# Kernel tuning notes

Measured on AMD Instinct MI355X. Metric: run time of the kernel, lower is better.

## Reference

```python
import jax, jax.numpy as jnp
import numpy as np

SAMPLE_POINTS = 1000
THRESH = 0.1
MAX_RATIO = 0.1
BIG = 1e9


def _sobel_boundary(mask):
    # mask: [B, H, W] -> boundary magnitude [B, H, W]
    kx = jnp.array([[-1, 0, 1], [-2, 0, 2], [-1, 0, 1]], jnp.float32).reshape(1, 1, 3, 3)
    ky = jnp.array([[-1, -2, -1], [0, 0, 0], [1, 2, 1]], jnp.float32).reshape(1, 1, 3, 3)
    x = mask[:, None, :, :]
    dn = ('NCHW', 'OIHW', 'NCHW')
    gx = jax.lax.conv_general_dilated(x, kx, (1, 1), [(1, 1), (1, 1)], dimension_numbers=dn)
    gy = jax.lax.conv_general_dilated(x, ky, (1, 1), [(1, 1), (1, 1)], dimension_numbers=dn)
    return jnp.sqrt(gx * gx + gy * gy + 1e-8)[:, 0]


def _extract_points(bmap, keys, H, W):
    # bmap: [B, H, W]. Returns points [B, P, 2] float and validity mask [B, P].
    # Torch version uses torch.where + randperm subsampling; here we pick a
    # uniformly-random subset of valid boundary pixels via noisy top_k
    # (fixed-shape, jit-compatible stream compaction).
    def one(bm, key):
        flat = bm.reshape(-1)
        valid = flat > THRESH
        noise = jax.random.uniform(key, flat.shape)
        score = valid.astype(jnp.float32) * 2.0 + noise  # valid in (2,3), invalid in (0,1)
        _, idx = jax.lax.top_k(score, SAMPLE_POINTS)
        pts = jnp.stack([(idx // W).astype(jnp.float32), (idx % W).astype(jnp.float32)], axis=-1)
        pvalid = valid[idx]
        has_any = valid.any()
        # empty-boundary fallback: single center point (like torch version)
        center = jnp.array([H // 2, W // 2], jnp.float32)
        pts = jnp.where(has_any, pts, jnp.broadcast_to(center, pts.shape))
        pvalid = jnp.where(has_any, pvalid, jnp.arange(SAMPLE_POINTS) == 0)
        return pts, pvalid

    return jax.vmap(one)(bmap, keys)


def _hausdorff(pp, pv, tp, tv, diag):
    # pp: [B,P,2], tp: [B,T,2]; masked symmetric Hausdorff per batch element.
    pp2 = jnp.sum(pp * pp, -1)  # [B,P]
    tp2 = jnp.sum(tp * tp, -1)  # [B,T]
    d2 = pp2[:, :, None] + tp2[:, None, :] - 2.0 * jnp.einsum('bpc,btc->bpt', pp, tp)
    D = jnp.sqrt(jnp.maximum(d2, 0.0))  # [B,P,T]
    min_p2t = jnp.min(jnp.where(tv[:, None, :], D, BIG), axis=2)  # [B,P]
    a = jnp.max(jnp.where(pv, min_p2t, -BIG), axis=1)  # [B]
    min_t2p = jnp.min(jnp.where(pv[:, :, None], D, BIG), axis=1)  # [B,T]
    b = jnp.max(jnp.where(tv, min_t2p, -BIG), axis=1)  # [B]
    hd = jnp.maximum(a, b) / diag
    return jnp.clip(hd, 0.0, MAX_RATIO)


def setup_inputs() -> dict:
    key = jax.random.key(0)
    k1, k2 = jax.random.split(key)
    B, H, W = 64, 512, 512
    pred_logits = jax.random.normal(k1, (B, H, W), dtype=jnp.float32)
    target = (jax.random.uniform(k2, (B, H, W)) > 0.5).astype(jnp.float32)
    return {"pred_logits": pred_logits, "target": target}


def reference(pred_logits, target):
    B, H, W = pred_logits.shape
    pred_probs = jax.nn.sigmoid(pred_logits)
    bmap_pred = _sobel_boundary(pred_probs)
    bmap_tgt = _sobel_boundary(target)
    keys = jax.random.split(jax.random.key(1), 2 * B)
    pp, pv = _extract_points(bmap_pred, keys[:B], H, W)
    tp, tv = _extract_points(bmap_tgt, keys[B:], H, W)
    diag = jnp.sqrt(jnp.float32(H * H + W * W))
    hd = _hausdorff(pp, pv, tp, tv, diag)  # [B]
    return jnp.mean(hd)
```

## Files before the change

### kernel.cpp

```cpp
#include <hip/hip_runtime.h>
#include <stdint.h>


#define HH 512
#define WW 512
#define NPIX (HH * WW)
#define NSEL 1000
#define SLICE_CAP 320
#define CUTM (253u << 14)
#define BITCUT ((((253u << 15) - 1u)) << 9)
#define ROWS_PER 32

#if __has_builtin(__builtin_amdgcn_alignbit)
__device__ __forceinline__ uint32_t rotl32(uint32_t x, int r) {
  return __builtin_amdgcn_alignbit(x, x, (32 - r) & 31);
}
#else
__device__ __forceinline__ uint32_t rotl32(uint32_t x, int r) {
  return (x << r) | (x >> (32 - r));
}
#endif

__device__ __forceinline__ void tf2x32(uint32_t k0, uint32_t k1,
                                       uint32_t c0, uint32_t c1,
                                       uint32_t& o0, uint32_t& o1) {
  uint32_t ks2 = k0 ^ k1 ^ 0x1BD11BDAu;
  uint32_t x0 = c0 + k0, x1 = c1 + k1;
#define TF_R(r) { x0 += x1; x1 = rotl32(x1, (r)); x1 ^= x0; }
  TF_R(13) TF_R(15) TF_R(26) TF_R(6)
  x0 += k1;  x1 += ks2 + 1u;
  TF_R(17) TF_R(29) TF_R(16) TF_R(24)
  x0 += ks2; x1 += k0 + 2u;
  TF_R(13) TF_R(15) TF_R(26) TF_R(6)
  x0 += k0;  x1 += k1 + 3u;
  TF_R(17) TF_R(29) TF_R(16) TF_R(24)
  x0 += k1;  x1 += ks2 + 4u;
  TF_R(13) TF_R(15) TF_R(26) TF_R(6)
  x0 += ks2; x1 += k0 + 5u;
#undef TF_R
  o0 = x0; o1 = x1;
}

__device__ __forceinline__ uint32_t tf_bits(uint32_t k0, uint32_t k1, uint32_t p) {
  uint32_t ks2 = k0 ^ k1 ^ 0x1BD11BDAu;
  uint32_t x0 = k0, x1 = p + k1;
#define TF_R(r) { x0 += x1; x1 = rotl32(x1, (r)); x1 ^= x0; }
  TF_R(13) TF_R(15) TF_R(26) TF_R(6)
  x0 += k1;  x1 += ks2 + 1u;
  TF_R(17) TF_R(29) TF_R(16) TF_R(24)
  x0 += ks2; x1 += k0 + 2u;
  TF_R(13) TF_R(15) TF_R(26) TF_R(6)
  x0 += k0;  x1 += k1 + 3u;
  TF_R(17) TF_R(29) TF_R(16) TF_R(24)
  x0 += k1;  x1 += ks2 + 4u;
  TF_R(13) TF_R(15) TF_R(26) TF_R(6)
  x0 += ks2; x1 += k0 + 5u;
#undef TF_R
  return x0 ^ x1;
}

__device__ __forceinline__ uint32_t m_from_bits(uint32_t bits) {
  float noise = __uint_as_float((bits >> 9) | 0x3F800000u) - 1.0f;
  float score = 2.0f + noise;
  return __float_as_uint(score) - 0x40000000u;
}

__device__ __forceinline__ uint32_t pixel_m(uint32_t k0, uint32_t k1, int p) {
  uint32_t b1, b2;
  tf2x32(k0, k1, 0u, (uint32_t)p, b1, b2);
  return m_from_bits(b1 ^ b2);
}

__device__ __forceinline__ float sigf(float x) { return 1.0f / (1.0f + __expf(-x)); }

__device__ __forceinline__ float ldval(const float* __restrict__ img, int r, int c, bool isPred) {
  if (r < 0 || r > HH - 1 || c < 0 || c > WW - 1) return 0.0f;
  float v = img[(size_t)r * WW + c];
  return isPred ? sigf(v) : v;
}

__device__ __forceinline__ uint32_t pack_pt(uint32_t p) {
  return ((p >> 9) << 16) | (p & 511u);
}

template <bool PRED>
__device__ __forceinline__ void load_row10(const float* __restrict__ img, int rn,
                                           int lane, float v[10]) {
  if ((unsigned)rn < (unsigned)HH) {
    const float* rp = img + ((size_t)rn << 9) + (lane << 3);
    float4 x = *(const float4*)rp;
    float4 y = *(const float4*)(rp + 4);
    if (PRED) {
      x.x = sigf(x.x); x.y = sigf(x.y); x.z = sigf(x.z); x.w = sigf(x.w);
      y.x = sigf(y.x); y.y = sigf(y.y); y.z = sigf(y.z); y.w = sigf(y.w);
    }
    v[1] = x.x; v[2] = x.y; v[3] = x.z; v[4] = x.w;
    v[5] = y.x; v[6] = y.y; v[7] = y.z; v[8] = y.w;
    float l = __shfl_up(y.w, 1);
    float r = __shfl_down(x.x, 1);
    v[0] = (lane == 0) ? 0.0f : l;
    v[9] = (lane == 63) ? 0.0f : r;
  } else {
#pragma unroll
    for (int i = 0; i < 10; ++i) v[i] = 0.0f;
  }
}

template <bool PRED>
__device__ __forceinline__ void sobel_body(const float* __restrict__ img, int b,
                                           int slice, int t,
                                           unsigned long long* stage, int* s_cn,
                                           int* s_cv) {
  const int lane = t & 63, w = t >> 6;
  const int rbase = slice * ROWS_PER + 8 * w;
  uint32_t k0, k1;
  tf2x32(0u, 1u, 0u, (uint32_t)b, k0, k1);

  float A[10], B_[10], C_[10], D_[10], E_[10], F_[10];
  load_row10<PRED>(img, rbase - 1, lane, A);
  load_row10<PRED>(img, rbase, lane, B_);

  int cnt = 0;
  uint32_t prow = (uint32_t)((rbase << 9) + (lane << 3));

  auto do_row = [&](const float (&P)[10], const float (&Q)[10], const float (&R)[10],
                    uint32_t prow_r) {
    uint32_t bits[8];
#pragma unroll
    for (int j = 0; j < 8; ++j) bits[j] = tf_bits(k0, k1, prow_r + (uint32_t)j);
    float da[10], e[10];
#pragma unroll
    for (int k = 0; k < 10; ++k) {
      da[k] = R[k] - P[k];
      e[k] = P[k] + 2.0f * Q[k] + R[k];
    }
    uint32_t vldmask = 0, candmask = 0;
#pragma unroll
    for (int j = 0; j < 8; ++j) {
      float gx = e[j + 2] - e[j];
      float gy = da[j] + 2.0f * da[j + 1] + da[j + 2];
      bool vld = (gx * gx + gy * gy + 1e-8f) > 0.01f;
      vldmask |= (vld ? 1u : 0u) << j;
      candmask |= ((vld && bits[j] >= BITCUT) ? 1u : 0u) << j;
    }
    cnt += __popc(vldmask);
    while (candmask) {
      int j = __ffs(candmask) - 1;
      candmask &= candmask - 1;
      uint32_t m = m_from_bits(bits[j]);
      int i = atomicAdd(s_cn, 1);
      if (i < SLICE_CAP)
        stage[i] = ((unsigned long long)m << 32) | (prow_r + (uint32_t)j);
    }
  };

#pragma unroll
  for (int g = 0; g < 2; ++g) {
    const int r = rbase + 4 * g;
    load_row10<PRED>(img, r + 1, lane, C_);
    load_row10<PRED>(img, r + 2, lane, D_);
    load_row10<PRED>(img, r + 3, lane, E_);
    load_row10<PRED>(img, r + 4, lane, F_);
    do_row(A, B_, C_, prow);
    do_row(B_, C_, D_, prow + 512);
    do_row(C_, D_, E_, prow + 1024);
    do_row(D_, E_, F_, prow + 1536);
    if (g == 0) {
#pragma unroll
      for (int k = 0; k < 10; ++k) { A[k] = E_[k]; B_[k] = F_[k]; }
      prow += 2048;
    }
  }
#pragma unroll
  for (int o = 32; o > 0; o >>= 1) cnt += __shfl_down(cnt, o);
  if (lane == 0) atomicAdd(s_cv, cnt);
}

__global__ __launch_bounds__(256, 4) void sobel_cand(
    const float* __restrict__ pred, const float* __restrict__ tgt,
    int2* __restrict__ g_scnt, unsigned long long* __restrict__ g_cand) {
  const int bid = blockIdx.x;
  const int b = bid >> 4, s = bid & 15;
  const int t = threadIdx.x;
  __shared__ unsigned long long stage[SLICE_CAP];
  __shared__ int s_cn, s_cv;
  if (t == 0) { s_cn = 0; s_cv = 0; }
  __syncthreads();
  if (b < 64) sobel_body<true>(pred + (size_t)b * NPIX, b, s, t, stage, &s_cn, &s_cv);
  else        sobel_body<false>(tgt + (size_t)(b - 64) * NPIX, b, s, t, stage, &s_cn, &s_cv);
  __syncthreads();
  const int raw = s_cn;
  const int n = raw < SLICE_CAP ? raw : SLICE_CAP;
  for (int i = t; i < n; i += 256) g_cand[(size_t)bid * SLICE_CAP + i] = stage[i];
  if (t == 0) g_scnt[bid] = make_int2(s_cv, raw);
}

__global__ __launch_bounds__(256) void resolve_kernel(
    const float* __restrict__ pred, const float* __restrict__ tgt,
    const int2* __restrict__ g_scnt, unsigned long long* __restrict__ g_cand,
    uint32_t* __restrict__ g_pts, int* __restrict__ g_counts) {
  const int img = blockIdx.x;
  const int t = threadIdx.x;

  __shared__ int segc[16];
  __shared__ int s_info[4];
  __shared__ int ch[256];
  __shared__ int fh[1024];
  __shared__ int aux[256];
  __shared__ unsigned long long ties[256];
  __shared__ int s_pos, s_nt, s_T1, s_r1, s_T2, s_r2;

  if (t == 0) {
    int cv = 0, hi = 0, ovf = 0;
    for (int s = 0; s < 16; ++s) {
      int2 v = g_scnt[img * 16 + s];
      cv += v.x;
      hi += v.y;
      segc[s] = v.y < SLICE_CAP ? v.y : SLICE_CAP;
      if (v.y > SLICE_CAP) ovf = 1;
    }
    s_info[0] = cv; s_info[1] = hi; s_info[2] = ovf;
    s_pos = 0; s_nt = 0;
  }
  __syncthreads();
  const int cv = s_info[0];
  if (cv == 0) {
    if (t == 0) { g_pts[img * NSEL] = (256u << 16) | 256u; g_counts[img] = 1; }
    return;
  }
  const int need = cv < NSEL ? cv : NSEL;
  bool slow = (s_info[2] != 0) || (s_info[1] < need);

  unsigned long long* C = g_cand + (size_t)img * 16 * SLICE_CAP;
  int ncand;

  if (slow) {
    const bool isPred = img < 64;
    const float* im = isPred ? pred + (size_t)img * NPIX : tgt + (size_t)(img - 64) * NPIX;
    uint32_t k0, k1;
    tf2x32(0u, 1u, 0u, (uint32_t)img, k0, k1);
    ch[t] = 0;
    __syncthreads();
    for (int p = t; p < NPIX; p += 256) {
      int r = p >> 9, c = p & 511;
      float gx = (ldval(im, r - 1, c + 1, isPred) - ldval(im, r - 1, c - 1, isPred)) +
                 2.0f * (ldval(im, r, c + 1, isPred) - ldval(im, r, c - 1, isPred)) +
                 (ldval(im, r + 1, c + 1, isPred) - ldval(im, r + 1, c - 1, isPred));
      float gy = (ldval(im, r + 1, c - 1, isPred) - ldval(im, r - 1, c - 1, isPred)) +
                 2.0f * (ldval(im, r + 1, c, isPred) - ldval(im, r - 1, c, isPred)) +
                 (ldval(im, r + 1, c + 1, isPred) - ldval(im, r - 1, c + 1, isPred));
      if ((gx * gx + gy * gy + 1e-8f) > 0.01f) {
        uint32_t m = pixel_m(k0, k1, p);
        uint32_t cb = m >> 14; if (cb > 255u) cb = 255u;
        atomicAdd(&ch[cb], 1);
      }
    }
    __syncthreads();
    {
      aux[t] = ch[t];
      __syncthreads();
      for (int o = 1; o < 256; o <<= 1) {
        int v = (t + o < 256) ? aux[t + o] : 0;
        __syncthreads();
        aux[t] += v;
        __syncthreads();
      }
      int nx = (t + 1 < 256) ? aux[t + 1] : 0;
      if (aux[t] >= need && nx < need) s_T1 = t;
      __syncthreads();
    }
    const uint32_t Tc = (uint32_t)s_T1;
    if (t == 0) s_info[3] = 0;
    __syncthreads();
    for (int p = t; p < NPIX; p += 256) {
      int r = p >> 9, c = p & 511;
      float gx = (ldval(im, r - 1, c + 1, isPred) - ldval(im, r - 1, c - 1, isPred)) +
                 2.0f * (ldval(im, r, c + 1, isPred) - ldval(im, r, c - 1, isPred)) +
                 (ldval(im, r + 1, c + 1, isPred) - ldval(im, r + 1, c - 1, isPred));
      float gy = (ldval(im, r + 1, c - 1, isPred) - ldval(im, r - 1, c - 1, isPred)) +
                 2.0f * (ldval(im, r + 1, c, isPred) - ldval(im, r - 1, c, isPred)) +
                 (ldval(im, r + 1, c + 1, isPred) - ldval(im, r - 1, c + 1, isPred));
      if ((gx * gx + gy * gy + 1e-8f) > 0.01f) {
        uint32_t m = pixel_m(k0, k1, p);
        uint32_t cb = m >> 14; if (cb > 255u) cb = 255u;
        if (cb >= Tc) {
          int i = atomicAdd(&s_info[3], 1);
          if (i < 16 * SLICE_CAP) C[i] = ((unsigned long long)m << 32) | (uint32_t)p;
        }
      }
    }
    __syncthreads();
    ncand = s_info[3] < 16 * SLICE_CAP ? s_info[3] : 16 * SLICE_CAP;
    if (t == 0) { segc[0] = ncand; for (int s = 1; s < 16; ++s) segc[s] = 0; }
    __syncthreads();
  }

  ch[t] = 0;
  for (int i = t; i < 1024; i += 256) fh[i] = 0;
  __syncthreads();
  for (int s = 0; s < 16; ++s) {
    const unsigned long long* seg = C + (size_t)s * SLICE_CAP;
    for (int i = t; i < segc[s]; i += 256) {
      uint32_t m = (uint32_t)(seg[i] >> 32);
      uint32_t cb = m >> 14; if (cb > 255u) cb = 255u;
      atomicAdd(&ch[cb], 1);
    }
  }
  __syncthreads();
  {
    aux[t] = ch[t];
    __syncthreads();
    for (int o = 1; o < 256; o <<= 1) {
      int v = (t + o < 256) ? aux[t + o] : 0;
      __syncthreads();
      aux[t] += v;
      __syncthreads();
    }
    int nx = (t + 1 < 256) ? aux[t + 1] : 0;
    if (aux[t] >= need && nx < need) { s_T1 = t; s_r1 = need - nx; }
    __syncthreads();
  }
  const uint32_t T1 = (uint32_t)s_T1;
  const int r1 = s_r1;
  const uint32_t baseM = T1 << 14;

  for (int s = 0; s < 16; ++s) {
    const unsigned long long* seg = C + (size_t)s * SLICE_CAP;
    for (int i = t; i < segc[s]; i += 256) {
      unsigned long long e = seg[i];
      uint32_t m = (uint32_t)(e >> 32), p = (uint32_t)e;
      uint32_t cb = m >> 14; if (cb > 255u) cb = 255u;
      if (cb > T1) {
        int pos = atomicAdd(&s_pos, 1);
        g_pts[img * NSEL + pos] = pack_pt(p);
      } else if (cb == T1) {
        uint32_t f = (m - baseM) >> 4; if (f > 1023u) f = 1023u;
        atomicAdd(&fh[f], 1);
      }
    }
  }
  __syncthreads();
  {
    int base = 4 * t, sv = 0;
    for (int j = 3; j >= 0; --j) { sv += fh[base + j]; fh[base + j] = sv; }
    aux[t] = sv;
    __syncthreads();
    for (int o = 1; o < 256; o <<= 1) {
      int v = (t + o < 256) ? aux[t + o] : 0;
      __syncthreads();
      aux[t] += v;
      __syncthreads();
    }
    int add = (t < 255) ? aux[t + 1] : 0;
    for (int j = 0; j < 4; ++j) fh[base + j] += add;
    __syncthreads();
    for (int j = 0; j < 4; ++j) {
      int idx = base + j;
      int sfx = fh[idx];
      int nx = (idx < 1023) ? fh[idx + 1] : 0;
      if (sfx >= r1 && nx < r1) { s_T2 = idx; s_r2 = r1 - nx; }
    }
    __syncthreads();
  }
  const int T2 = s_T2, r2 = s_r2;
  for (int s = 0; s < 16; ++s) {
    const unsigned long long* seg = C + (size_t)s * SLICE_CAP;
    for (int i = t; i < segc[s]; i += 256) {
      unsigned long long e = seg[i];
      uint32_t m = (uint32_t)(e >> 32), p = (uint32_t)e;
      uint32_t cb = m >> 14; if (cb > 255u) cb = 255u;
      if (cb == T1) {
        uint32_t f = (m - baseM) >> 4; if (f > 1023u) f = 1023u;
        if ((int)f > T2) {
          int pos = atomicAdd(&s_pos, 1);
          g_pts[img * NSEL + pos] = pack_pt(p);
        } else if ((int)f == T2) {
          int j = atomicAdd(&s_nt, 1);
          if (j < 256) ties[j] = e;
        }
      }
    }
  }
  __syncthreads();
  int nt = s_nt < 256 ? s_nt : 256;
  for (int i = t; i < nt; i += 256) {
    unsigned long long e = ties[i];
    uint32_t mi = (uint32_t)(e >> 32), pi = (uint32_t)e;
    int rank = 0;
    for (int j = 0; j < nt; ++j) {
      unsigned long long e2 = ties[j];
      uint32_t mj = (uint32_t)(e2 >> 32), pj = (uint32_t)e2;
      rank += (mj > mi) || (mj == mi && pj < pi);
    }
    if (rank < r2) {
      int pos = atomicAdd(&s_pos, 1);
      g_pts[img * NSEL + pos] = pack_pt(pi);
    }
  }
  __syncthreads();
  if (t == 0) g_counts[img] = s_pos;
}

__global__ __launch_bounds__(256) void haus_kernel(
    const uint32_t* __restrict__ g_pts, const int* __restrict__ g_counts,
    float* __restrict__ g_hpart) {
  const int bid = blockIdx.x;
  const int img = bid >> 3;
  const int dir = (bid >> 2) & 1;
  const int seg = bid & 3;
  const int t = threadIdx.x;
  const int iOwn = dir ? 64 + img : img;
  const int iOth = dir ? img : 64 + img;
  const int nOwn = g_counts[iOwn];
  const int nOth = g_counts[iOth];
  __shared__ float2 o[NSEL];
  __shared__ float red[256];
  for (int i = t; i < nOth; i += 256) {
    uint32_t v = g_pts[iOth * NSEL + i];
    o[i] = make_float2((float)(v >> 16), (float)(v & 0xFFFFu));
  }
  __syncthreads();
  float best = 0.0f;
  const int lo = seg * 250;
  const int hi = min(nOwn, lo + 250);
  for (int i = lo + t; i < hi; i += 256) {
    uint32_t v = g_pts[iOwn * NSEL + i];
    float pr = (float)(v >> 16), pc = (float)(v & 0xFFFFu);
    float mn0 = 3.4e38f, mn1 = 3.4e38f, mn2 = 3.4e38f, mn3 = 3.4e38f;
    int j = 0;
    for (; j + 3 < nOth; j += 4) {
      float dr0 = pr - o[j].x,     dc0 = pc - o[j].y;
      float dr1 = pr - o[j + 1].x, dc1 = pc - o[j + 1].y;
      float dr2 = pr - o[j + 2].x, dc2 = pc - o[j + 2].y;
      float dr3 = pr - o[j + 3].x, dc3 = pc - o[j + 3].y;
      mn0 = fminf(mn0, dr0 * dr0 + dc0 * dc0);
      mn1 = fminf(mn1, dr1 * dr1 + dc1 * dc1);
      mn2 = fminf(mn2, dr2 * dr2 + dc2 * dc2);
      mn3 = fminf(mn3, dr3 * dr3 + dc3 * dc3);
    }
    for (; j < nOth; ++j) {
      float dr = pr - o[j].x, dc = pc - o[j].y;
      mn0 = fminf(mn0, dr * dr + dc * dc);
    }
    float mn = fminf(fminf(mn0, mn1), fminf(mn2, mn3));
    best = fmaxf(best, mn);
  }
  red[t] = best;
  __syncthreads();
  for (int st = 128; st > 0; st >>= 1) {
    if (t < st) red[t] = fmaxf(red[t], red[t + st]);
    __syncthreads();
  }
  if (t == 0) g_hpart[bid] = red[0];
}

__global__ __launch_bounds__(64) void fin_kernel(const float* __restrict__ g_hpart,
                                                 float* __restrict__ out) {
  const int t = threadIdx.x;
  float mx = 0.0f;
  for (int j = 0; j < 8; ++j) mx = fmaxf(mx, g_hpart[t * 8 + j]);
  float diag = sqrtf((float)(HH * HH + WW * WW));
  float hd = sqrtf(fmaxf(mx, 0.0f)) / diag;
  hd = fminf(fmaxf(hd, 0.0f), 0.1f);
  float s = hd;
  for (int o = 32; o > 0; o >>= 1) s += __shfl_down(s, o);
  if (t == 0) out[0] = s * 0.015625f;
}

#define WS_SCNT   0u
#define WS_COUNTS 16384u
#define WS_HPART  (WS_COUNTS + 512u)
#define WS_PTS    (WS_HPART + 2048u)
#define WS_CAND   (WS_PTS + 512000u)

extern "C" void kernel_launch(void* const* d_in, const int* in_sizes, int n_in,
                              void* d_out, int out_size, void* d_ws, size_t ws_size,
                              hipStream_t stream) {
  const float* pred = (const float*)d_in[0];
  const float* tgt = (const float*)d_in[1];
  float* out = (float*)d_out;
  char* ws = (char*)d_ws;
  int2* g_scnt = (int2*)(ws + WS_SCNT);
  int* g_counts = (int*)(ws + WS_COUNTS);
  float* g_hpart = (float*)(ws + WS_HPART);
  uint32_t* g_pts = (uint32_t*)(ws + WS_PTS);
  unsigned long long* g_cand = (unsigned long long*)(ws + WS_CAND);

  sobel_cand<<<2048, 256, 0, stream>>>(pred, tgt, g_scnt, g_cand);
  resolve_kernel<<<128, 256, 0, stream>>>(pred, tgt, g_scnt, g_cand, g_pts, g_counts);
  haus_kernel<<<512, 256, 0, stream>>>(g_pts, g_counts, g_hpart);
  fin_kernel<<<1, 64, 0, stream>>>(g_hpart, out);
}
```

Before: 244.3 us.

## Software-pipeline Sobel row loads with rotating three-row buffer

Result: no change. 243.9 us (-0.2%).

```diff
diff --git a/kernel.cpp b/kernel.cpp
--- a/kernel.cpp
+++ b/kernel.cpp
@@ -81,29 +81,6 @@
 
 __device__ __forceinline__ uint32_t pack_pt(uint32_t p) {
   return ((p >> 9) << 16) | (p & 511u);
-}
-
-template <bool PRED>
-__device__ __forceinline__ void load_row10(const float* __restrict__ img, int rn,
-                                           int lane, float v[10]) {
-  if ((unsigned)rn < (unsigned)HH) {
-    const float* rp = img + ((size_t)rn << 9) + (lane << 3);
-    float4 x = *(const float4*)rp;
-    float4 y = *(const float4*)(rp + 4);
-    if (PRED) {
-      x.x = sigf(x.x); x.y = sigf(x.y); x.z = sigf(x.z); x.w = sigf(x.w);
-      y.x = sigf(y.x); y.y = sigf(y.y); y.z = sigf(y.z); y.w = sigf(y.w);
-    }
-    v[1] = x.x; v[2] = x.y; v[3] = x.z; v[4] = x.w;
-    v[5] = y.x; v[6] = y.y; v[7] = y.z; v[8] = y.w;
-    float l = __shfl_up(y.w, 1);
-    float r = __shfl_down(x.x, 1);
-    v[0] = (lane == 0) ? 0.0f : l;
-    v[9] = (lane == 63) ? 0.0f : r;
-  } else {
-#pragma unroll
-    for (int i = 0; i < 10; ++i) v[i] = 0.0f;
-  }
 }
 
 template <bool PRED>
@@ -115,35 +92,74 @@
   const int rbase = slice * ROWS_PER + 8 * w;
   uint32_t k0, k1;
   tf2x32(0u, 1u, 0u, (uint32_t)b, k0, k1);
-
-  float A[10], B_[10], C_[10], D_[10], E_[10], F_[10];
-  load_row10<PRED>(img, rbase - 1, lane, A);
-  load_row10<PRED>(img, rbase, lane, B_);
-
+  k0 = __builtin_amdgcn_readfirstlane(k0);
+  k1 = __builtin_amdgcn_readfirstlane(k1);
+
+  float4 ra[3], rb[3];
+  float v[3][10];
   int cnt = 0;
-  uint32_t prow = (uint32_t)((rbase << 9) + (lane << 3));
-
-  auto do_row = [&](const float (&P)[10], const float (&Q)[10], const float (&R)[10],
-                    uint32_t prow_r) {
+  const uint32_t pbase = (uint32_t)((rbase << 9) + (lane << 3));
+
+  auto load_raw = [&](int s, int rn) {
+    if ((unsigned)rn < (unsigned)HH) {
+      const float* rp = img + ((size_t)rn << 9) + (lane << 3);
+      ra[s] = *(const float4*)rp;
+      rb[s] = *(const float4*)(rp + 4);
+    }
+  };
+  auto promote = [&](int s, int rn) {
+    float (&vv)[10] = v[s];
+    if ((unsigned)rn < (unsigned)HH) {
+      float4 x = ra[s], y = rb[s];
+      if (PRED) {
+        x.x = sigf(x.x); x.y = sigf(x.y); x.z = sigf(x.z); x.w = sigf(x.w);
+        y.x = sigf(y.x); y.y = sigf(y.y); y.z = sigf(y.z); y.w = sigf(y.w);
+      }
+      vv[1] = x.x; vv[2] = x.y; vv[3] = x.z; vv[4] = x.w;
+      vv[5] = y.x; vv[6] = y.y; vv[7] = y.z; vv[8] = y.w;
+      float l = __shfl_up(y.w, 1);
+      float r = __shfl_down(x.x, 1);
+      vv[0] = (lane == 0) ? 0.0f : l;
+      vv[9] = (lane == 63) ? 0.0f : r;
+    } else {
+#pragma unroll
+      for (int i = 0; i < 10; ++i) vv[i] = 0.0f;
+    }
+  };
+
+  load_raw(0, rbase - 1);
+  load_raw(1, rbase);
+  load_raw(2, rbase + 1);
+  promote(0, rbase - 1);
+  promote(1, rbase);
+
+#pragma unroll
+  for (int r = 0; r < 8; ++r) {
+    load_raw(r % 3, rbase + r + 2);
+
+    const uint32_t prow_r = pbase + (uint32_t)(r << 9);
     uint32_t bits[8];
 #pragma unroll
     for (int j = 0; j < 8; ++j) bits[j] = tf_bits(k0, k1, prow_r + (uint32_t)j);
+
+    promote((r + 2) % 3, rbase + r + 1);
+
+    const int ip = r % 3, iq = (r + 1) % 3, ir = (r + 2) % 3;
     float da[10], e[10];
 #pragma unroll
     for (int k = 0; k < 10; ++k) {
-      da[k] = R[k] - P[k];
-      e[k] = P[k] + 2.0f * Q[k] + R[k];
-    }
-    uint32_t vldmask = 0, candmask = 0;
+      da[k] = v[ir][k] - v[ip][k];
+      e[k] = v[ip][k] + 2.0f * v[iq][k] + v[ir][k];
+    }
+    uint32_t candmask = 0;
 #pragma unroll
     for (int j = 0; j < 8; ++j) {
       float gx = e[j + 2] - e[j];
       float gy = da[j] + 2.0f * da[j + 1] + da[j + 2];
       bool vld = (gx * gx + gy * gy + 1e-8f) > 0.01f;
-      vldmask |= (vld ? 1u : 0u) << j;
+      cnt += vld ? 1 : 0;
       candmask |= ((vld && bits[j] >= BITCUT) ? 1u : 0u) << j;
     }
-    cnt += __popc(vldmask);
     while (candmask) {
       int j = __ffs(candmask) - 1;
       candmask &= candmask - 1;
@@ -151,24 +167,6 @@
       int i = atomicAdd(s_cn, 1);
       if (i < SLICE_CAP)
         stage[i] = ((unsigned long long)m << 32) | (prow_r + (uint32_t)j);
-    }
-  };
-
-#pragma unroll
-  for (int g = 0; g < 2; ++g) {
-    const int r = rbase + 4 * g;
-    load_row10<PRED>(img, r + 1, lane, C_);
-    load_row10<PRED>(img, r + 2, lane, D_);
-    load_row10<PRED>(img, r + 3, lane, E_);
-    load_row10<PRED>(img, r + 4, lane, F_);
-    do_row(A, B_, C_, prow);
-    do_row(B_, C_, D_, prow + 512);
-    do_row(C_, D_, E_, prow + 1024);
-    do_row(D_, E_, F_, prow + 1536);
-    if (g == 0) {
-#pragma unroll
-      for (int k = 0; k < 10; ++k) { A[k] = E_[k]; B_[k] = F_[k]; }
-      prow += 2048;
     }
   }
 #pragma unroll
```
